# Performance work log

Measured on AMD Instinct MI355X. Metric: run time of the kernel, lower is better.

## Reference

```python
import jax, jax.numpy as jnp
import numpy as np

D_MODEL = 1024
NUM_HEADS = 16
D_K = D_MODEL // NUM_HEADS


def setup_inputs() -> dict:
    key = jax.random.key(0)
    ks = jax.random.split(key, 7)
    B, S = 4, 2048
    lim = float(np.sqrt(6.0 / (D_MODEL + D_MODEL)))  # xavier uniform
    x = jax.random.normal(ks[0], (B, S, D_MODEL), dtype=jnp.float32)
    w_q = jax.random.uniform(ks[1], (D_MODEL, D_MODEL), jnp.float32, -lim, lim)
    w_k = jax.random.uniform(ks[2], (D_MODEL, D_MODEL), jnp.float32, -lim, lim)
    w_v = jax.random.uniform(ks[3], (D_MODEL, D_MODEL), jnp.float32, -lim, lim)
    w_o = jax.random.uniform(ks[4], (D_MODEL, D_MODEL), jnp.float32, -lim, lim)
    b_o = jnp.zeros((D_MODEL,), jnp.float32)
    ln_g = jnp.ones((D_MODEL,), jnp.float32)
    ln_b = jnp.zeros((D_MODEL,), jnp.float32)
    return {"x": x, "w_q": w_q, "w_k": w_k, "w_v": w_v, "w_o": w_o,
            "b_o": b_o, "ln_g": ln_g, "ln_b": ln_b}


def _layer_norm(y, g, b, eps=1e-5):
    mu = jnp.mean(y, axis=-1, keepdims=True)
    var = jnp.var(y, axis=-1, keepdims=True)
    return (y - mu) * jax.lax.rsqrt(var + eps) * g + b


def reference(x, w_q, w_k, w_v, w_o, b_o, ln_g, ln_b):
    B, S, D = x.shape
    # Linear weights stored torch-style [out, in]: y = x @ W^T
    def proj(w):
        return jnp.einsum('bsd,ed->bse', x, w).reshape(B, S, NUM_HEADS, D_K).transpose(0, 2, 1, 3)
    Q, K, V = proj(w_q), proj(w_k), proj(w_v)  # [B, H, S, d_k]
    scores = jnp.einsum('bhqd,bhkd->bhqk', Q, K) / jnp.sqrt(jnp.float32(D_K))
    attn = jax.nn.softmax(scores, axis=-1)  # dropout identity at eval
    out = jnp.einsum('bhqk,bhkd->bhqd', attn, V)  # [B, H, S, d_k]
    out = out.transpose(0, 2, 1, 3).reshape(B, S, D)
    out = jnp.einsum('bsd,ed->bse', out, w_o) + b_o
    return _layer_norm(x + out, ln_g, ln_b)
```

## Files before the change

### kernel.cpp

```cpp
#include <hip/hip_runtime.h>

typedef __bf16 bf16;
typedef bf16 v8bf __attribute__((ext_vector_type(8)));
typedef bf16 v4bf __attribute__((ext_vector_type(4)));
typedef float v4f __attribute__((ext_vector_type(4)));
typedef float v16f __attribute__((ext_vector_type(16)));
typedef unsigned int u32;
typedef u32 v4u __attribute__((ext_vector_type(4)));

#define GAS __attribute__((address_space(1)))
#define LAS __attribute__((address_space(3)))

constexpr int D    = 1024;
constexpr int ROWS = 8192;

__global__ __launch_bounds__(256) void cast_all(
    const float* __restrict__ x,
    const float* __restrict__ wq, const float* __restrict__ wk,
    const float* __restrict__ wv, const float* __restrict__ wo,
    bf16* __restrict__ xb, bf16* __restrict__ wqb, bf16* __restrict__ wkb,
    bf16* __restrict__ wvb, bf16* __restrict__ wob)
{
    int i = blockIdx.x * 256 + threadIdx.x;
    const float* src; bf16* dst; int off;
    if (i < 2 * 1024 * 1024) { src = x; dst = xb; off = i; }
    else {
        int j = i - 2 * 1024 * 1024;
        int w = j >> 18;
        off = j & ((1 << 18) - 1);
        src = (w == 0) ? wq : (w == 1) ? wk : (w == 2) ? wv : wo;
        dst = (w == 0) ? wqb : (w == 1) ? wkb : (w == 2) ? wvb : wob;
    }
    float4 v = ((const float4*)src)[off];
    v4bf o;
    o[0] = (bf16)v.x; o[1] = (bf16)v.y; o[2] = (bf16)v.z; o[3] = (bf16)v.w;
    ((v4bf*)dst)[off] = o;
}

template<int MODE, int NTN>
__global__ __launch_bounds__(512, 2) void gemm8(
    const bf16* __restrict__ A, const bf16* __restrict__ W,
    bf16* __restrict__ Oq, bf16* __restrict__ Ok, bf16* __restrict__ Ov,
    float* __restrict__ Of, const float* __restrict__ bias,
    const float* __restrict__ X)
{
    __shared__ bf16 Abuf[3][256 * 64];
    __shared__ bf16 Bbuf[3][128 * 64];

    const int id   = blockIdx.x;
    const int wgid = (id & 7) * (4 * NTN) + (id >> 3);
    const int mT   = wgid / NTN;
    const int nT   = wgid - mT * NTN;
    const long rowA0 = (long)mT * 256;
    const long colB0 = (long)nT * 128;

    const int tid  = threadIdx.x;
    const int lane = tid & 63;
    const int wave = tid >> 6;
    const int quad = lane >> 4;
    const int l16  = lane & 15;
    const int wm   = (wave >> 1) * 64;
    const int wn   = (wave & 1) * 64;

    const int srow = wave * 8 + (lane >> 3);
    const int scol = ((lane & 7) ^ (lane >> 3)) * 8;
    const bf16* gA = A + (rowA0 + srow) * D + scol;
    const bf16* gB = W + (colB0 + srow) * D + scol;
    const int dstOff = wave * 512;

    auto stage = [&](int bi, int t) {
        const bf16* a = gA + (long)t * 64;
        const bf16* b = gB + (long)t * 64;
        #pragma unroll
        for (int i = 0; i < 4; i++)
            __builtin_amdgcn_global_load_lds(
                (const GAS void*)(a + (long)i * 64 * D),
                (LAS void*)(&Abuf[bi][i * 4096 + dstOff]), 16, 0, 0);
        #pragma unroll
        for (int i = 0; i < 2; i++)
            __builtin_amdgcn_global_load_lds(
                (const GAS void*)(b + (long)i * 64 * D),
                (LAS void*)(&Bbuf[bi][i * 4096 + dstOff]), 16, 0, 0);
    };

    const v4f vzero = {0.f, 0.f, 0.f, 0.f};
    v4f acc[4][4];
    #pragma unroll
    for (int i = 0; i < 4; i++)
        #pragma unroll
        for (int j = 0; j < 4; j++) acc[i][j] = vzero;

    int sa[2], sb[2];
    #pragma unroll
    for (int ks = 0; ks < 2; ks++) {
        const int ch = ((ks * 4 + quad) ^ (l16 & 7)) * 8;
        sa[ks] = (wm + l16) * 64 + ch;
        sb[ks] = (wn + l16) * 64 + ch;
    }

    auto compute = [&](int bi) {
        const bf16* As = &Abuf[bi][0];
        const bf16* Bs = &Bbuf[bi][0];
        v8bf af[2][4], bf[2][4];
        #pragma unroll
        for (int ks = 0; ks < 2; ks++) {
            #pragma unroll
            for (int mi = 0; mi < 4; mi++)
                af[ks][mi] = *(const v8bf*)(As + sa[ks] + mi * 1024);
            #pragma unroll
            for (int ni = 0; ni < 4; ni++)
                bf[ks][ni] = *(const v8bf*)(Bs + sb[ks] + ni * 1024);
        }
        __builtin_amdgcn_s_setprio(1);
        #pragma unroll
        for (int ks = 0; ks < 2; ks++)
            #pragma unroll
            for (int mi = 0; mi < 4; mi++)
                #pragma unroll
                for (int ni = 0; ni < 4; ni++)
                    acc[mi][ni] = __builtin_amdgcn_mfma_f32_16x16x32_bf16(
                        af[ks][mi], bf[ks][ni], acc[mi][ni], 0, 0, 0);
        __builtin_amdgcn_s_setprio(0);
    };

    constexpr int NT = 16;
    stage(0, 0);
    stage(1, 1);
    asm volatile("s_waitcnt vmcnt(6)" ::: "memory");
    __builtin_amdgcn_s_barrier();

    for (int t = 0; t < NT; ++t) {
        if (t + 2 < NT) stage((t + 2) % 3, t + 2);
        compute(t % 3);
        if (t + 1 < NT) {
            if (t + 2 < NT) {
                asm volatile("s_waitcnt vmcnt(6)" ::: "memory");
            } else {
                asm volatile("s_waitcnt vmcnt(0)" ::: "memory");
            }
            __builtin_amdgcn_s_barrier();
        }
    }

    const float qscale = 0.125f * 1.44269504f;

    if (MODE == 0) {
        const int z = (int)(colB0 >> 10);
        #pragma unroll
        for (int mi = 0; mi < 4; mi++) {
            #pragma unroll
            for (int ni = 0; ni < 4; ni++) {
                const long col = colB0 + wn + ni * 16 + l16;
                const long c   = col & 1023;
                const long row0 = rowA0 + wm + mi * 16 + quad * 4;
                if (z == 2) {
                    const long h_ = c >> 6, dd = c & 63;
                    const long b_ = row0 >> 11, s0 = row0 & 2047;
                    v4bf pk;
                    #pragma unroll
                    for (int r = 0; r < 4; r++) pk[r] = (bf16)acc[mi][ni][r];
                    *(v4bf*)(Ov + ((b_ * 16 + h_) * 64 + dd) * 2048 + s0) = pk;
                } else {
                    bf16* Ob = (z == 0) ? Oq : Ok;
                    #pragma unroll
                    for (int r = 0; r < 4; r++) {
                        float v = acc[mi][ni][r];
                        if (z == 0) v *= qscale;
                        Ob[(row0 + r) * D + c] = (bf16)v;
                    }
                }
            }
        }
    } else {
        #pragma unroll
        for (int mi = 0; mi < 4; mi++) {
            #pragma unroll
            for (int ni = 0; ni < 4; ni++) {
                const long col = colB0 + wn + ni * 16 + l16;
                const float bv = bias[col];
                #pragma unroll
                for (int r = 0; r < 4; r++) {
                    const long row = rowA0 + wm + mi * 16 + quad * 4 + r;
                    Of[row * D + col] = acc[mi][ni][r] + bv + X[row * D + col];
                }
            }
        }
    }
}

__global__ __launch_bounds__(512, 4) void attn_kernel(
    const bf16* __restrict__ Q, const bf16* __restrict__ Kg,
    const bf16* __restrict__ VtG, bf16* __restrict__ O)
{
    const int id  = blockIdx.x;
    const int xcd = id & 7, j = id >> 3;
    const int qt  = j & 7;
    const int g   = xcd + 8 * (j >> 3);
    const int h   = g & 15, b = g >> 4;

    const int tid  = threadIdx.x;
    const int lane = tid & 63;
    const int wave = tid >> 6;
    const int l31  = lane & 31;
    const int hi   = lane >> 5;

    __shared__ bf16 Kt[4][64 * 64];
    __shared__ bf16 Vt[4][64 * 64];

    const long qrow = (long)(b * 2048 + qt * 256 + wave * 32 + l31);
    v8bf qB[4];
    #pragma unroll
    for (int f = 0; f < 4; f++)
        qB[f] = *(const v8bf*)(Q + qrow * D + h * 64 + f * 16 + hi * 8);

    const v16f z16 = {0.f,0.f,0.f,0.f,0.f,0.f,0.f,0.f,
                      0.f,0.f,0.f,0.f,0.f,0.f,0.f,0.f};
    v16f o_acc[2];
    o_acc[0] = z16; o_acc[1] = z16;
    float l0 = 0.f, l1 = 0.f;

    const int iR = tid >> 3;
    const int c8 = tid & 7;
    const bf16* kLane = Kg  + (long)b * 2048 * D + h * 64 + c8 * 8 + (long)iR * D;
    const bf16* vLane = VtG + (long)(b * 16 + h) * 64 * 2048 + c8 * 8 + (long)iR * 2048;
    const int wOff = iR * 64 + ((c8 ^ (iR & 7)) * 8);

    v8bf kp[2], vp[2];
    kp[0] = *(const v8bf*)(kLane); vp[0] = *(const v8bf*)(vLane);
    kLane += 64 * D; vLane += 64;
    kp[1] = *(const v8bf*)(kLane); vp[1] = *(const v8bf*)(vLane);
    kLane += 64 * D; vLane += 64;
    *(v8bf*)(&Kt[0][wOff]) = kp[0]; *(v8bf*)(&Vt[0][wOff]) = vp[0];
    *(v8bf*)(&Kt[1][wOff]) = kp[1]; *(v8bf*)(&Vt[1][wOff]) = vp[1];
    kp[0] = *(const v8bf*)(kLane); vp[0] = *(const v8bf*)(vLane);
    kLane += 64 * D; vLane += 64;
    kp[1] = *(const v8bf*)(kLane); vp[1] = *(const v8bf*)(vLane);
    kLane += 64 * D; vLane += 64;

    auto compute = [&](const int bq) {
        #pragma unroll
        for (int ko = 0; ko < 2; ko++) {
            const int krow = ko * 32 + l31;
            const int ksw  = krow & 7;
            v8bf kA[4];
            #pragma unroll
            for (int f = 0; f < 4; f++)
                kA[f] = *(const v8bf*)(&Kt[bq][krow * 64 + (((2 * f + hi) ^ ksw) * 8)]);
            __builtin_amdgcn_s_setprio(1);
            v16f st = __builtin_amdgcn_mfma_f32_32x32x16_bf16(kA[0], qB[0], z16, 0, 0, 0);
            st = __builtin_amdgcn_mfma_f32_32x32x16_bf16(kA[1], qB[1], st, 0, 0, 0);
            st = __builtin_amdgcn_mfma_f32_32x32x16_bf16(kA[2], qB[2], st, 0, 0, 0);
            st = __builtin_amdgcn_mfma_f32_32x32x16_bf16(kA[3], qB[3], st, 0, 0, 0);
            __builtin_amdgcn_s_setprio(0);

            float p[16];
            #pragma unroll
            for (int r = 0; r < 16; r++) {
                p[r] = __builtin_amdgcn_exp2f(st[r]);
                if (r & 1) l1 += p[r]; else l0 += p[r];
            }

            #pragma unroll
            for (int u = 0; u < 2; u++) {
                const int s = ko * 2 + u;
                u32 a0, a1, b0, b1;
                asm("v_cvt_pk_bf16_f32 %0, %1, %2" : "=v"(a0) : "v"(p[u*8+0]), "v"(p[u*8+1]));
                asm("v_cvt_pk_bf16_f32 %0, %1, %2" : "=v"(a1) : "v"(p[u*8+2]), "v"(p[u*8+3]));
                asm("v_cvt_pk_bf16_f32 %0, %1, %2" : "=v"(b0) : "v"(p[u*8+4]), "v"(p[u*8+5]));
                asm("v_cvt_pk_bf16_f32 %0, %1, %2" : "=v"(b1) : "v"(p[u*8+6]), "v"(p[u*8+7]));
                asm("v_permlane32_swap_b32 %0, %1" : "+v"(a0), "+v"(b0));
                asm("v_permlane32_swap_b32 %0, %1" : "+v"(a1), "+v"(b1));
                v4u w; w[0] = a0; w[1] = a1; w[2] = b0; w[3] = b1;
                const v8bf pa = __builtin_bit_cast(v8bf, w);
                const int vsw = (l31 & 7);
                v8bf vb0 = *(const v8bf*)(&Vt[bq][(l31)      * 64 + (((2 * s + hi) ^ vsw) * 8)]);
                v8bf vb1 = *(const v8bf*)(&Vt[bq][(32 + l31) * 64 + (((2 * s + hi) ^ vsw) * 8)]);
                __builtin_amdgcn_s_setprio(1);
                o_acc[0] = __builtin_amdgcn_mfma_f32_32x32x16_bf16(pa, vb0, o_acc[0], 0, 0, 0);
                o_acc[1] = __builtin_amdgcn_mfma_f32_32x32x16_bf16(pa, vb1, o_acc[1], 0, 0, 0);
                __builtin_amdgcn_s_setprio(0);
            }
        }
    };

    for (int gg = 0; gg < 16; ++gg) {
        const int cb = (gg & 1) * 2;
        __syncthreads();

        if (gg < 15) {
            *(v8bf*)(&Kt[cb ^ 2][wOff])       = kp[0];
            *(v8bf*)(&Vt[cb ^ 2][wOff])       = vp[0];
            *(v8bf*)(&Kt[(cb ^ 2) + 1][wOff]) = kp[1];
            *(v8bf*)(&Vt[(cb ^ 2) + 1][wOff]) = vp[1];
        }
        if (gg < 14) {
            kp[0] = *(const v8bf*)(kLane); vp[0] = *(const v8bf*)(vLane);
            kLane += 64 * D; vLane += 64;
            kp[1] = *(const v8bf*)(kLane); vp[1] = *(const v8bf*)(vLane);
            kLane += 64 * D; vLane += 64;
        }

        compute(cb);
        compute(cb + 1);
    }

    float l_acc = l0 + l1;
    l_acc += __shfl_xor(l_acc, 32);

    const long obase = (long)(b * 2048 + qt * 256 + wave * 32);
    #pragma unroll
    for (int r = 0; r < 16; r++) {
        const int qp = (r & 3) + 8 * (r >> 2) + 4 * hi;
        const float inv = 1.f / __shfl(l_acc, qp);
        O[(obase + qp) * D + h * 64 + l31]      = (bf16)(o_acc[0][r] * inv);
        O[(obase + qp) * D + h * 64 + 32 + l31] = (bf16)(o_acc[1][r] * inv);
    }
}

__global__ __launch_bounds__(256) void ln_kernel(
    const float* __restrict__ g, const float* __restrict__ beta,
    float* __restrict__ out)
{
    const int row = blockIdx.x;
    const int t = threadIdx.x;
    const int lane = t & 63, wave = t >> 6;
    const long base = (long)row * D + t * 4;

    float4 yv = *(const float4*)(out + base);
    float y0 = yv.x, y1 = yv.y, y2 = yv.z, y3 = yv.w;
    float s1 = y0 + y1 + y2 + y3;
    float s2 = y0*y0 + y1*y1 + y2*y2 + y3*y3;
    #pragma unroll
    for (int off = 1; off < 64; off <<= 1) {
        s1 += __shfl_xor(s1, off);
        s2 += __shfl_xor(s2, off);
    }
    __shared__ float r1[4], r2[4];
    if (lane == 0) { r1[wave] = s1; r2[wave] = s2; }
    __syncthreads();
    float S1 = r1[0] + r1[1] + r1[2] + r1[3];
    float S2 = r2[0] + r2[1] + r2[2] + r2[3];
    float mu  = S1 * (1.f / 1024.f);
    float var = S2 * (1.f / 1024.f) - mu * mu;
    float rsd = rsqrtf(var + 1e-5f);

    float4 gv = *(const float4*)(g + t * 4);
    float4 bv = *(const float4*)(beta + t * 4);
    float4 o;
    o.x = (y0 - mu) * rsd * gv.x + bv.x;
    o.y = (y1 - mu) * rsd * gv.y + bv.y;
    o.z = (y2 - mu) * rsd * gv.z + bv.z;
    o.w = (y3 - mu) * rsd * gv.w + bv.w;
    *(float4*)(out + base) = o;
}

extern "C" void kernel_launch(void* const* d_in, const int* in_sizes, int n_in,
                              void* d_out, int out_size, void* d_ws, size_t ws_size,
                              hipStream_t stream)
{
    const float* x   = (const float*)d_in[0];
    const float* wq  = (const float*)d_in[1];
    const float* wk  = (const float*)d_in[2];
    const float* wv  = (const float*)d_in[3];
    const float* wo  = (const float*)d_in[4];
    const float* bo  = (const float*)d_in[5];
    const float* lng = (const float*)d_in[6];
    const float* lnb = (const float*)d_in[7];
    float* out = (float*)d_out;

    char* ws = (char*)d_ws;
    bf16* xb  = (bf16*)(ws);
    bf16* wqb = (bf16*)(ws + (size_t)16 * 1024 * 1024);
    bf16* wkb = wqb + 1024 * 1024;
    bf16* wvb = wkb + 1024 * 1024;
    bf16* wob = wvb + 1024 * 1024;
    bf16* Qb  = (bf16*)(ws + (size_t)24 * 1024 * 1024);
    bf16* Kb  = Qb + (size_t)ROWS * D;
    bf16* VtG = Kb + (size_t)ROWS * D;
    bf16* Ab  = VtG + (size_t)ROWS * D;

    cast_all<<<12288, 256, 0, stream>>>(x, wq, wk, wv, wo,
                                        xb, wqb, wkb, wvb, wob);

    gemm8<0, 24><<<768, 512, 0, stream>>>(xb, wqb, Qb, Kb, VtG,
                                          nullptr, nullptr, nullptr);

    attn_kernel<<<dim3(512, 1, 1), 512, 0, stream>>>(Qb, Kb, VtG, Ab);

    gemm8<1, 8><<<256, 512, 0, stream>>>(Ab, wob, nullptr, nullptr, nullptr,
                                         out, bo, x);

    ln_kernel<<<8192, 256, 0, stream>>>(lng, lnb, out);
}
```

Before: 299.8 us.

## Interleave global-to-LDS prefetch with per-k-slice MFMA phases in QKV GEMM

Restructures the triple-buffered GEMM main loop so each k-tile is split into two k-slice phases. Each phase does its LDS fragment reads, issues half of the next-next tile's global_load_lds, then runs the MFMAs under a sched_barrier with raised priority. This interleaves load issue with compute the way ping-pong schedules do. It adds extra barriers per tile, two or four instead of one, which may add sync overhead. Register pressure drops because only one k-slice of fragments is live at a time.

```diff
diff --git a/kernel.cpp b/kernel.cpp
--- a/kernel.cpp
+++ b/kernel.cpp
@@ -68,21 +68,6 @@
     const bf16* gB = W + (colB0 + srow) * D + scol;
     const int dstOff = wave * 512;
 
-    auto stage = [&](int bi, int t) {
-        const bf16* a = gA + (long)t * 64;
-        const bf16* b = gB + (long)t * 64;
-        #pragma unroll
-        for (int i = 0; i < 4; i++)
-            __builtin_amdgcn_global_load_lds(
-                (const GAS void*)(a + (long)i * 64 * D),
-                (LAS void*)(&Abuf[bi][i * 4096 + dstOff]), 16, 0, 0);
-        #pragma unroll
-        for (int i = 0; i < 2; i++)
-            __builtin_amdgcn_global_load_lds(
-                (const GAS void*)(b + (long)i * 64 * D),
-                (LAS void*)(&Bbuf[bi][i * 4096 + dstOff]), 16, 0, 0);
-    };
-
     const v4f vzero = {0.f, 0.f, 0.f, 0.f};
     v4f acc[4][4];
     #pragma unroll
@@ -98,46 +83,84 @@
         sb[ks] = (wn + l16) * 64 + ch;
     }
 
-    auto compute = [&](int bi) {
+    auto stage_full = [&](int bi, int t) {
+        const bf16* a = gA + (long)t * 64;
+        const bf16* b = gB + (long)t * 64;
+        #pragma unroll
+        for (int i = 0; i < 4; i++)
+            __builtin_amdgcn_global_load_lds(
+                (const GAS void*)(a + (long)i * 64 * D),
+                (LAS void*)(&Abuf[bi][i * 4096 + dstOff]), 16, 0, 0);
+        #pragma unroll
+        for (int i = 0; i < 2; i++)
+            __builtin_amdgcn_global_load_lds(
+                (const GAS void*)(b + (long)i * 64 * D),
+                (LAS void*)(&Bbuf[bi][i * 4096 + dstOff]), 16, 0, 0);
+    };
+
+    constexpr int NT = 16;
+    stage_full(0, 0);
+    stage_full(1, 1);
+    asm volatile("s_waitcnt vmcnt(6)" ::: "memory");
+    __builtin_amdgcn_s_barrier();
+
+    for (int t = 0; t < NT; ++t) {
+        const int bi = t % 3;
+        const int bs = (t + 2) % 3;
         const bf16* As = &Abuf[bi][0];
         const bf16* Bs = &Bbuf[bi][0];
-        v8bf af[2][4], bf[2][4];
-        #pragma unroll
-        for (int ks = 0; ks < 2; ks++) {
+        #pragma unroll
+        for (int ks = 0; ks < 2; ++ks) {
+            v8bf af[4], bf4[4];
             #pragma unroll
             for (int mi = 0; mi < 4; mi++)
-                af[ks][mi] = *(const v8bf*)(As + sa[ks] + mi * 1024);
+                af[mi] = *(const v8bf*)(As + sa[ks] + mi * 1024);
             #pragma unroll
             for (int ni = 0; ni < 4; ni++)
-                bf[ks][ni] = *(const v8bf*)(Bs + sb[ks] + ni * 1024);
-        }
-        __builtin_amdgcn_s_setprio(1);
-        #pragma unroll
-        for (int ks = 0; ks < 2; ks++)
+                bf4[ni] = *(const v8bf*)(Bs + sb[ks] + ni * 1024);
+
+            if (t + 2 < NT) {
+                const bf16* a2 = gA + (long)(t + 2) * 64;
+                const bf16* b2 = gB + (long)(t + 2) * 64;
+                if (ks == 0) {
+                    __builtin_amdgcn_global_load_lds(
+                        (const GAS void*)(a2),
+                        (LAS void*)(&Abuf[bs][dstOff]), 16, 0, 0);
+                    __builtin_amdgcn_global_load_lds(
+                        (const GAS void*)(a2 + (long)64 * D),
+                        (LAS void*)(&Abuf[bs][4096 + dstOff]), 16, 0, 0);
+                    __builtin_amdgcn_global_load_lds(
+                        (const GAS void*)(b2),
+                        (LAS void*)(&Bbuf[bs][dstOff]), 16, 0, 0);
+                } else {
+                    __builtin_amdgcn_global_load_lds(
+                        (const GAS void*)(a2 + (long)128 * D),
+                        (LAS void*)(&Abuf[bs][2 * 4096 + dstOff]), 16, 0, 0);
+                    __builtin_amdgcn_global_load_lds(
+                        (const GAS void*)(a2 + (long)192 * D),
+                        (LAS void*)(&Abuf[bs][3 * 4096 + dstOff]), 16, 0, 0);
+                    __builtin_amdgcn_global_load_lds(
+                        (const GAS void*)(b2 + (long)64 * D),
+                        (LAS void*)(&Bbuf[bs][4096 + dstOff]), 16, 0, 0);
+                }
+            }
+
+            if (ks == 1 && t + 1 < NT) {
+                if (t + 2 < NT) asm volatile("s_waitcnt vmcnt(6)" ::: "memory");
+                else            asm volatile("s_waitcnt vmcnt(0)" ::: "memory");
+            }
+
+            __builtin_amdgcn_s_barrier();
+            asm volatile("s_waitcnt lgkmcnt(0)" ::: "memory");
+            __builtin_amdgcn_sched_barrier(0);
+            __builtin_amdgcn_s_setprio(1);
             #pragma unroll
             for (int mi = 0; mi < 4; mi++)
                 #pragma unroll
                 for (int ni = 0; ni < 4; ni++)
                     acc[mi][ni] = __builtin_amdgcn_mfma_f32_16x16x32_bf16(
-                        af[ks][mi], bf[ks][ni], acc[mi][ni], 0, 0, 0);
-        __builtin_amdgcn_s_setprio(0);
-    };
-
-    constexpr int NT = 16;
-    stage(0, 0);
-    stage(1, 1);
-    asm volatile("s_waitcnt vmcnt(6)" ::: "memory");
-    __builtin_amdgcn_s_barrier();
-
-    for (int t = 0; t < NT; ++t) {
-        if (t + 2 < NT) stage((t + 2) % 3, t + 2);
-        compute(t % 3);
-        if (t + 1 < NT) {
-            if (t + 2 < NT) {
-                asm volatile("s_waitcnt vmcnt(6)" ::: "memory");
-            } else {
-                asm volatile("s_waitcnt vmcnt(0)" ::: "memory");
-            }
+                        af[mi], bf4[ni], acc[mi][ni], 0, 0, 0);
+            __builtin_amdgcn_s_setprio(0);
             __builtin_amdgcn_s_barrier();
         }
     }
```

Result: faster. 278.6 us (-7.1%).

## Use 256x256 tiles for QKV GEMM and shrink K-step to 32

Applied to the files above, without the earlier changes.

Replaces the templated QKV projection GEMM with a dedicated kernel using 256x256 output tiles per workgroup. Each wave holds an 8x4 accumulator grid, and the A and B loads are split so the B staging overlaps the second half of the MFMA work. The output-projection GEMM now uses a 32-wide K step with a new XOR swizzle and claims 4 workgroups per CU in its launch bounds. This is meant to raise operand reuse and cut global traffic, at the cost of twice as many barrier-separated iterations and higher register pressure.

```diff
diff --git a/kernel.cpp b/kernel.cpp
--- a/kernel.cpp
+++ b/kernel.cpp
@@ -37,15 +37,161 @@
     ((v4bf*)dst)[off] = o;
 }
 
-template<int MODE, int NTN>
-__global__ __launch_bounds__(512, 2) void gemm8(
+__global__ __launch_bounds__(512, 2) void gemmq(
     const bf16* __restrict__ A, const bf16* __restrict__ W,
-    bf16* __restrict__ Oq, bf16* __restrict__ Ok, bf16* __restrict__ Ov,
+    bf16* __restrict__ Oq, bf16* __restrict__ Ok, bf16* __restrict__ Ov)
+{
+    __shared__ bf16 Abuf[3][256 * 32];
+    __shared__ bf16 Bbuf[3][256 * 32];
+
+    const int id   = blockIdx.x;
+    const int wgid = (id & 7) * 48 + (id >> 3);
+    const int mT   = wgid / 12;
+    const int nT   = wgid - mT * 12;
+    const long rowA0 = (long)mT * 256;
+    const long colB0 = (long)nT * 256;
+
+    const int tid  = threadIdx.x;
+    const int lane = tid & 63;
+    const int wave = tid >> 6;
+    const int quad = lane >> 4;
+    const int l16  = lane & 15;
+    const int wr   = wave >> 2;
+    const int wc   = wave & 3;
+
+    const int rS   = tid >> 2;
+    const int cS   = tid & 3;
+    const int colS = ((cS ^ ((rS >> 1) & 3)) * 8);
+    const bf16* gA = A + (rowA0 + rS) * D + colS;
+    const bf16* gB = W + (colB0 + rS) * D + colS;
+    const int dstOff = wave * 512;
+
+    const v4f vzero = {0.f, 0.f, 0.f, 0.f};
+    v4f acc[8][4];
+    #pragma unroll
+    for (int i = 0; i < 8; i++)
+        #pragma unroll
+        for (int j = 0; j < 4; j++) acc[i][j] = vzero;
+
+    const int rsw = (quad ^ ((l16 >> 1) & 3)) * 8;
+    int sa[8], sb[4];
+    #pragma unroll
+    for (int i = 0; i < 8; i++)
+        sa[i] = (wr * 128 + i * 16 + l16) * 32 + rsw;
+    #pragma unroll
+    for (int i = 0; i < 4; i++)
+        sb[i] = (wc * 64 + i * 16 + l16) * 32 + rsw;
+
+    auto stageA = [&](int bi, int t) {
+        __builtin_amdgcn_global_load_lds(
+            (const GAS void*)(gA + (long)t * 32),
+            (LAS void*)(&Abuf[bi][dstOff]), 16, 0, 0);
+        __builtin_amdgcn_global_load_lds(
+            (const GAS void*)(gA + (long)128 * D + (long)t * 32),
+            (LAS void*)(&Abuf[bi][4096 + dstOff]), 16, 0, 0);
+    };
+    auto stageB = [&](int bi, int t) {
+        __builtin_amdgcn_global_load_lds(
+            (const GAS void*)(gB + (long)t * 32),
+            (LAS void*)(&Bbuf[bi][dstOff]), 16, 0, 0);
+        __builtin_amdgcn_global_load_lds(
+            (const GAS void*)(gB + (long)128 * D + (long)t * 32),
+            (LAS void*)(&Bbuf[bi][4096 + dstOff]), 16, 0, 0);
+    };
+
+    constexpr int NT = 32;
+    stageA(0, 0); stageB(0, 0);
+    stageA(1, 1); stageB(1, 1);
+    asm volatile("s_waitcnt vmcnt(4)" ::: "memory");
+    __builtin_amdgcn_s_barrier();
+
+    for (int t = 0; t < NT; ++t) {
+        const int bi = t % 3;
+        const int bs = (t + 2) % 3;
+        const bf16* As = &Abuf[bi][0];
+        const bf16* Bs = &Bbuf[bi][0];
+
+        v8bf af[4], bfr[4];
+        #pragma unroll
+        for (int i = 0; i < 4; i++) af[i]  = *(const v8bf*)(As + sa[i]);
+        #pragma unroll
+        for (int i = 0; i < 4; i++) bfr[i] = *(const v8bf*)(Bs + sb[i]);
+        if (t + 2 < NT) stageA(bs, t + 2);
+
+        __builtin_amdgcn_s_barrier();
+        asm volatile("s_waitcnt lgkmcnt(0)" ::: "memory");
+        __builtin_amdgcn_sched_barrier(0);
+        __builtin_amdgcn_s_setprio(1);
+        #pragma unroll
+        for (int mi = 0; mi < 4; mi++)
+            #pragma unroll
+            for (int ni = 0; ni < 4; ni++)
+                acc[mi][ni] = __builtin_amdgcn_mfma_f32_16x16x32_bf16(
+                    af[mi], bfr[ni], acc[mi][ni], 0, 0, 0);
+        __builtin_amdgcn_s_setprio(0);
+        __builtin_amdgcn_s_barrier();
+
+        v8bf ag[4];
+        #pragma unroll
+        for (int i = 0; i < 4; i++) ag[i] = *(const v8bf*)(As + sa[4 + i]);
+        if (t + 2 < NT) stageB(bs, t + 2);
+        if (t + 1 < NT) {
+            if (t + 2 < NT) asm volatile("s_waitcnt vmcnt(4)" ::: "memory");
+            else            asm volatile("s_waitcnt vmcnt(0)" ::: "memory");
+        }
+
+        __builtin_amdgcn_s_barrier();
+        asm volatile("s_waitcnt lgkmcnt(0)" ::: "memory");
+        __builtin_amdgcn_sched_barrier(0);
+        __builtin_amdgcn_s_setprio(1);
+        #pragma unroll
+        for (int mi = 0; mi < 4; mi++)
+            #pragma unroll
+            for (int ni = 0; ni < 4; ni++)
+                acc[4 + mi][ni] = __builtin_amdgcn_mfma_f32_16x16x32_bf16(
+                    ag[mi], bfr[ni], acc[4 + mi][ni], 0, 0, 0);
+        __builtin_amdgcn_s_setprio(0);
+        __builtin_amdgcn_s_barrier();
+    }
+
+    const float qscale = 0.125f * 1.44269504f;
+    const int z = nT >> 2;
+
+    #pragma unroll
+    for (int mi = 0; mi < 8; mi++) {
+        #pragma unroll
+        for (int ni = 0; ni < 4; ni++) {
+            const long col = colB0 + wc * 64 + ni * 16 + l16;
+            const long c   = col & 1023;
+            const long row0 = rowA0 + wr * 128 + mi * 16 + quad * 4;
+            if (z == 2) {
+                const long h_ = c >> 6, dd = c & 63;
+                const long b_ = row0 >> 11, s0 = row0 & 2047;
+                v4bf pk;
+                #pragma unroll
+                for (int r = 0; r < 4; r++) pk[r] = (bf16)acc[mi][ni][r];
+                *(v4bf*)(Ov + ((b_ * 16 + h_) * 64 + dd) * 2048 + s0) = pk;
+            } else {
+                bf16* Ob = (z == 0) ? Oq : Ok;
+                #pragma unroll
+                for (int r = 0; r < 4; r++) {
+                    float v = acc[mi][ni][r];
+                    if (z == 0) v *= qscale;
+                    Ob[(row0 + r) * D + c] = (bf16)v;
+                }
+            }
+        }
+    }
+}
+
+template<int NTN>
+__global__ __launch_bounds__(512, 4) void gemm8(
+    const bf16* __restrict__ A, const bf16* __restrict__ W,
     float* __restrict__ Of, const float* __restrict__ bias,
     const float* __restrict__ X)
 {
-    __shared__ bf16 Abuf[3][256 * 64];
-    __shared__ bf16 Bbuf[3][128 * 64];
+    __shared__ bf16 Abuf[3][256 * 32];
+    __shared__ bf16 Bbuf[3][128 * 32];
 
     const int id   = blockIdx.x;
     const int wgid = (id & 7) * (4 * NTN) + (id >> 3);
@@ -62,26 +208,12 @@
     const int wm   = (wave >> 1) * 64;
     const int wn   = (wave & 1) * 64;
 
-    const int srow = wave * 8 + (lane >> 3);
-    const int scol = ((lane & 7) ^ (lane >> 3)) * 8;
-    const bf16* gA = A + (rowA0 + srow) * D + scol;
-    const bf16* gB = W + (colB0 + srow) * D + scol;
+    const int rS   = tid >> 2;
+    const int cS   = tid & 3;
+    const int colS = ((cS ^ ((rS >> 1) & 3)) * 8);
+    const bf16* gA = A + (rowA0 + rS) * D + colS;
+    const bf16* gB = W + (colB0 + rS) * D + colS;
     const int dstOff = wave * 512;
-
-    auto stage = [&](int bi, int t) {
-        const bf16* a = gA + (long)t * 64;
-        const bf16* b = gB + (long)t * 64;
-        #pragma unroll
-        for (int i = 0; i < 4; i++)
-            __builtin_amdgcn_global_load_lds(
-                (const GAS void*)(a + (long)i * 64 * D),
-                (LAS void*)(&Abuf[bi][i * 4096 + dstOff]), 16, 0, 0);
-        #pragma unroll
-        for (int i = 0; i < 2; i++)
-            __builtin_amdgcn_global_load_lds(
-                (const GAS void*)(b + (long)i * 64 * D),
-                (LAS void*)(&Bbuf[bi][i * 4096 + dstOff]), 16, 0, 0);
-    };
 
     const v4f vzero = {0.f, 0.f, 0.f, 0.f};
     v4f acc[4][4];
@@ -90,99 +222,78 @@
         #pragma unroll
         for (int j = 0; j < 4; j++) acc[i][j] = vzero;
 
-    int sa[2], sb[2];
-    #pragma unroll
-    for (int ks = 0; ks < 2; ks++) {
-        const int ch = ((ks * 4 + quad) ^ (l16 & 7)) * 8;
-        sa[ks] = (wm + l16) * 64 + ch;
-        sb[ks] = (wn + l16) * 64 + ch;
-    }
-
-    auto compute = [&](int bi) {
+    const int rsw = (quad ^ ((l16 >> 1) & 3)) * 8;
+    int sa[4], sb[4];
+    #pragma unroll
+    for (int i = 0; i < 4; i++) {
+        sa[i] = (wm + i * 16 + l16) * 32 + rsw;
+        sb[i] = (wn + i * 16 + l16) * 32 + rsw;
+    }
+
+    auto stage = [&](int bi, int t) {
+        const bf16* a = gA + (long)t * 32;
+        const bf16* b = gB + (long)t * 32;
+        __builtin_amdgcn_global_load_lds(
+            (const GAS void*)(a),
+            (LAS void*)(&Abuf[bi][dstOff]), 16, 0, 0);
+        __builtin_amdgcn_global_load_lds(
+            (const GAS void*)(a + (long)128 * D),
+            (LAS void*)(&Abuf[bi][4096 + dstOff]), 16, 0, 0);
+        __builtin_amdgcn_global_load_lds(
+            (const GAS void*)(b),
+            (LAS void*)(&Bbuf[bi][dstOff]), 16, 0, 0);
+    };
+
+    constexpr int NT = 32;
+    stage(0, 0);
+    stage(1, 1);
+    asm volatile("s_waitcnt vmcnt(3)" ::: "memory");
+    __builtin_amdgcn_s_barrier();
+
+    for (int t = 0; t < NT; ++t) {
+        const int bi = t % 3;
         const bf16* As = &Abuf[bi][0];
         const bf16* Bs = &Bbuf[bi][0];
-        v8bf af[2][4], bf[2][4];
-        #pragma unroll
-        for (int ks = 0; ks < 2; ks++) {
-            #pragma unroll
-            for (int mi = 0; mi < 4; mi++)
-                af[ks][mi] = *(const v8bf*)(As + sa[ks] + mi * 1024);
+
+        v8bf af[4], bf4[4];
+        #pragma unroll
+        for (int mi = 0; mi < 4; mi++)
+            af[mi] = *(const v8bf*)(As + sa[mi]);
+        #pragma unroll
+        for (int ni = 0; ni < 4; ni++)
+            bf4[ni] = *(const v8bf*)(Bs + sb[ni]);
+
+        if (t + 2 < NT) stage((t + 2) % 3, t + 2);
+
+        if (t + 1 < NT) {
+            if (t + 2 < NT) asm volatile("s_waitcnt vmcnt(3)" ::: "memory");
+            else            asm volatile("s_waitcnt vmcnt(0)" ::: "memory");
+        }
+
+        __builtin_amdgcn_s_barrier();
+        asm volatile("s_waitcnt lgkmcnt(0)" ::: "memory");
+        __builtin_amdgcn_sched_barrier(0);
+        __builtin_amdgcn_s_setprio(1);
+        #pragma unroll
+        for (int mi = 0; mi < 4; mi++)
             #pragma unroll
             for (int ni = 0; ni < 4; ni++)
-                bf[ks][ni] = *(const v8bf*)(Bs + sb[ks] + ni * 1024);
-        }
-        __builtin_amdgcn_s_setprio(1);
-        #pragma unroll
-        for (int ks = 0; ks < 2; ks++)
-            #pragma unroll
-            for (int mi = 0; mi < 4; mi++)
-                #pragma unroll
-                for (int ni = 0; ni < 4; ni++)
-                    acc[mi][ni] = __builtin_amdgcn_mfma_f32_16x16x32_bf16(
-                        af[ks][mi], bf[ks][ni], acc[mi][ni], 0, 0, 0);
+                acc[mi][ni] = __builtin_amdgcn_mfma_f32_16x16x32_bf16(
+                    af[mi], bf4[ni], acc[mi][ni], 0, 0, 0);
         __builtin_amdgcn_s_setprio(0);
-    };
-
-    constexpr int NT = 16;
-    stage(0, 0);
-    stage(1, 1);
-    asm volatile("s_waitcnt vmcnt(6)" ::: "memory");
-    __builtin_amdgcn_s_barrier();
-
-    for (int t = 0; t < NT; ++t) {
-        if (t + 2 < NT) stage((t + 2) % 3, t + 2);
-        compute(t % 3);
-        if (t + 1 < NT) {
-            if (t + 2 < NT) {
-                asm volatile("s_waitcnt vmcnt(6)" ::: "memory");
-            } else {
-                asm volatile("s_waitcnt vmcnt(0)" ::: "memory");
-            }
-            __builtin_amdgcn_s_barrier();
-        }
-    }
-
-    const float qscale = 0.125f * 1.44269504f;
-
-    if (MODE == 0) {
-        const int z = (int)(colB0 >> 10);
-        #pragma unroll
-        for (int mi = 0; mi < 4; mi++) {
-            #pragma unroll
-            for (int ni = 0; ni < 4; ni++) {
-                const long col = colB0 + wn + ni * 16 + l16;
-                const long c   = col & 1023;
-                const long row0 = rowA0 + wm + mi * 16 + quad * 4;
-                if (z == 2) {
-                    const long h_ = c >> 6, dd = c & 63;
-                    const long b_ = row0 >> 11, s0 = row0 & 2047;
-                    v4bf pk;
-                    #pragma unroll
-                    for (int r = 0; r < 4; r++) pk[r] = (bf16)acc[mi][ni][r];
-                    *(v4bf*)(Ov + ((b_ * 16 + h_) * 64 + dd) * 2048 + s0) = pk;
-                } else {
-                    bf16* Ob = (z == 0) ? Oq : Ok;
-                    #pragma unroll
-                    for (int r = 0; r < 4; r++) {
-                        float v = acc[mi][ni][r];
-                        if (z == 0) v *= qscale;
-                        Ob[(row0 + r) * D + c] = (bf16)v;
-                    }
-                }
-            }
-        }
-    } else {
-        #pragma unroll
-        for (int mi = 0; mi < 4; mi++) {
-            #pragma unroll
-            for (int ni = 0; ni < 4; ni++) {
-                const long col = colB0 + wn + ni * 16 + l16;
-                const float bv = bias[col];
-                #pragma unroll
-                for (int r = 0; r < 4; r++) {
-                    const long row = rowA0 + wm + mi * 16 + quad * 4 + r;
-                    Of[row * D + col] = acc[mi][ni][r] + bv + X[row * D + col];
-                }
+        __builtin_amdgcn_s_barrier();
+    }
+
+    #pragma unroll
+    for (int mi = 0; mi < 4; mi++) {
+        #pragma unroll
+        for (int ni = 0; ni < 4; ni++) {
+            const long col = colB0 + wn + ni * 16 + l16;
+            const float bv = bias[col];
+            #pragma unroll
+            for (int r = 0; r < 4; r++) {
+                const long row = rowA0 + wm + mi * 16 + quad * 4 + r;
+                Of[row * D + col] = acc[mi][ni][r] + bv + X[row * D + col];
             }
         }
     }
@@ -382,13 +493,11 @@
     cast_all<<<12288, 256, 0, stream>>>(x, wq, wk, wv, wo,
                                         xb, wqb, wkb, wvb, wob);
 
-    gemm8<0, 24><<<768, 512, 0, stream>>>(xb, wqb, Qb, Kb, VtG,
-                                          nullptr, nullptr, nullptr);
+    gemmq<<<384, 512, 0, stream>>>(xb, wqb, Qb, Kb, VtG);
 
     attn_kernel<<<dim3(512, 1, 1), 512, 0, stream>>>(Qb, Kb, VtG, Ab);
 
-    gemm8<1, 8><<<256, 512, 0, stream>>>(Ab, wob, nullptr, nullptr, nullptr,
-                                         out, bo, x);
+    gemm8<8><<<256, 512, 0, stream>>>(Ab, wob, out, bo, x);
 
     ln_kernel<<<8192, 256, 0, stream>>>(lng, lnb, out);
 }
```

Result: slower. 310.0 us (+3.4%).
